# Performance work log

Hardware: AMD Instinct MI355X
Metric: run time of the kernel (lower is better)

The kernel has to match this reference:

```python
import jax, jax.numpy as jnp
import numpy as np

N_NODES = 100000
N_EDGES = 1600000
NEG_SLOPE = 0.2  # PyG GATConv default
BN_EPS = 1e-5


def gat_conv(x, src, dst, W, a_src, a_dst, bias):
    # x: [N, F], W: [F, H, C]
    h = jnp.einsum('nf,fhc->nhc', x, W)                 # [N, H, C]
    al_src = jnp.sum(h * a_src, axis=-1)                # [N, H]
    al_dst = jnp.sum(h * a_dst, axis=-1)                # [N, H]
    e = al_src[src] + al_dst[dst]                       # [E, H]
    e = jnp.where(e >= 0, e, NEG_SLOPE * e)             # leaky_relu(0.2)
    # segment softmax over incoming edges of each dst node
    emax = jax.ops.segment_max(e, dst, num_segments=N_NODES)
    ee = jnp.exp(e - emax[dst])
    denom = jax.ops.segment_sum(ee, dst, num_segments=N_NODES)
    alpha = ee / denom[dst]                             # [E, H]
    msg = alpha[:, :, None] * h[src]                    # [E, H, C]
    out = jax.ops.segment_sum(msg, dst, num_segments=N_NODES)  # [N, H, C]
    return out.mean(axis=1) + bias                      # concat=False -> head mean


def batch_norm(x, gamma, beta):
    mu = jnp.mean(x, axis=0)
    var = jnp.var(x, axis=0)  # biased, as in torch BN normalization
    return (x - mu) * jax.lax.rsqrt(var + BN_EPS) * gamma + beta


def setup_inputs() -> dict:
    key = jax.random.key(0)
    ks = jax.random.split(key, 16)
    inp = {
        'x': jax.random.normal(ks[0], (N_NODES, 128), jnp.float32),
        'edge_index': jax.random.randint(ks[1], (2, N_EDGES), 0, N_NODES, jnp.int64)
            if jax.config.jax_enable_x64 else
            jax.random.randint(ks[1], (2, N_EDGES), 0, N_NODES, jnp.int32),
        'edge_attr': jax.random.normal(ks[2], (N_EDGES, 8), jnp.float32),
        'W0': 0.1 * jax.random.normal(ks[3], (128, 4, 32), jnp.float32),
        'a_src0': 0.1 * jax.random.normal(ks[4], (4, 32), jnp.float32),
        'a_dst0': 0.1 * jax.random.normal(ks[5], (4, 32), jnp.float32),
        'b0': jnp.zeros((32,), jnp.float32),
        'g0': jnp.ones((32,), jnp.float32),
        'be0': jnp.zeros((32,), jnp.float32),
        'W1': 0.1 * jax.random.normal(ks[6], (32, 4, 32), jnp.float32),
        'a_src1': 0.1 * jax.random.normal(ks[7], (4, 32), jnp.float32),
        'a_dst1': 0.1 * jax.random.normal(ks[8], (4, 32), jnp.float32),
        'b1': jnp.zeros((32,), jnp.float32),
        'g1': jnp.ones((32,), jnp.float32),
        'be1': jnp.zeros((32,), jnp.float32),
        'W2': 0.1 * jax.random.normal(ks[9], (32, 4, 32), jnp.float32),
        'a_src2': 0.1 * jax.random.normal(ks[10], (4, 32), jnp.float32),
        'a_dst2': 0.1 * jax.random.normal(ks[11], (4, 32), jnp.float32),
        'b2': jnp.zeros((32,), jnp.float32),
    }
    return inp


def reference(x, edge_index, edge_attr, W0, a_src0, a_dst0, b0, g0, be0,
              W1, a_src1, a_dst1, b1, g1, be1, W2, a_src2, a_dst2, b2):
    src, dst = edge_index[0], edge_index[1]
    h = gat_conv(x, src, dst, W0, a_src0, a_dst0, b0)
    h = jax.nn.relu(batch_norm(h, g0, be0))  # dropout = identity (deterministic ref)
    h = gat_conv(h, src, dst, W1, a_src1, a_dst1, b1)
    h = jax.nn.relu(batch_norm(h, g1, be1))
    h = gat_conv(h, src, dst, W2, a_src2, a_dst2, b2)
    return (h, edge_attr)
```

## Files before the change

kernel.cpp:

```cpp
#include <hip/hip_runtime.h>
#include <cstdio>
#include <cstdint>

#define LRELU 0.2f
#define BN_EPS 1e-5f

typedef short bf16x8 __attribute__((ext_vector_type(8)));
typedef float f32x4 __attribute__((ext_vector_type(4)));

__device__ inline unsigned short f2bf(float f) {
  unsigned int u = __float_as_uint(f);
  u += 0x7fffu + ((u >> 16) & 1u);
  return (unsigned short)(u >> 16);
}
__device__ inline float bf2f(unsigned short v) {
  return __uint_as_float(((unsigned int)v) << 16);
}
__device__ inline float bflo(unsigned int u) { return __uint_as_float(u << 16); }
__device__ inline float bfhi(unsigned int u) { return __uint_as_float(u & 0xffff0000u); }


__global__ __launch_bounds__(256) void k_bhist_copy(const int* __restrict__ dst,
                                                    int* __restrict__ bh,
                                                    const float4* __restrict__ ea,
                                                    float4* __restrict__ oea,
                                                    int E) {
  __shared__ int cnt[512];
  for (int b = threadIdx.x; b < 512; b += 256) cnt[b] = 0;
  __syncthreads();
  const int gid = blockIdx.x * blockDim.x + threadIdx.x;
  const int gstride = gridDim.x * blockDim.x;
  for (int i = gid; i < E; i += gstride) atomicAdd(&cnt[dst[i] >> 8], 1);
  const int n4 = E * 2;
  for (int i = gid; i < n4; i += gstride) oea[i] = ea[i];
  __syncthreads();
  for (int b = threadIdx.x; b < 512; b += 256)
    if (cnt[b]) atomicAdd(&bh[b], cnt[b]);
}

__global__ __launch_bounds__(512) void k_exscan(const int* __restrict__ bh,
                                                int* __restrict__ bstart,
                                                int* __restrict__ bcur, int n,
                                                int* __restrict__ offsN) {
  __shared__ int sh[512];
  const int t = threadIdx.x;
  int v = (t < n) ? bh[t] : 0;
  sh[t] = v;
  __syncthreads();
  for (int s = 1; s < 512; s <<= 1) {
    int u = (t >= s) ? sh[t - s] : 0;
    __syncthreads();
    sh[t] += u;
    __syncthreads();
  }
  if (t < n) {
    int ex = sh[t] - v;
    bstart[t] = ex;
    bcur[t] = ex;
  }
  if (t == n - 1) {
    bstart[n] = sh[t];
    *offsN = sh[t];
  }
}

__global__ __launch_bounds__(256) void k_bscatter(const int* __restrict__ src,
                                                  const int* __restrict__ dst,
                                                  int* __restrict__ bcur,
                                                  uint2* __restrict__ bpair, int E) {
  __shared__ int cnt[512];
  const int chunk = (E + gridDim.x - 1) / gridDim.x;
  const int beg = blockIdx.x * chunk;
  const int end = min(E, beg + chunk);
  for (int b = threadIdx.x; b < 512; b += 256) cnt[b] = 0;
  __syncthreads();
  for (int e = beg + threadIdx.x; e < end; e += 256)
    atomicAdd(&cnt[dst[e] >> 8], 1);
  __syncthreads();
  for (int b = threadIdx.x; b < 512; b += 256) {
    int c = cnt[b];
    cnt[b] = (c > 0) ? atomicAdd(&bcur[b], c) : 0;
  }
  __syncthreads();
  for (int e = beg + threadIdx.x; e < end; e += 256) {
    int d = dst[e];
    int pos = atomicAdd(&cnt[d >> 8], 1);
    bpair[pos] = make_uint2((unsigned)src[e], (unsigned)d);
  }
}

__global__ __launch_bounds__(256) void k_bcsr2(const uint2* __restrict__ bpair,
                                               const int* __restrict__ bstart,
                                               int* __restrict__ offs,
                                               int* __restrict__ srcs, int N) {
  __shared__ int sc[256];
  __shared__ int cur[256];
  const int b = blockIdx.x;
  const int lo = b << 8;
  const int t = threadIdx.x;
  const int e0 = bstart[b], e1 = bstart[b + 1];
  sc[t] = 0;
  __syncthreads();
  for (int e = e0 + t; e < e1; e += 256) atomicAdd(&sc[bpair[e].y & 255], 1);
  __syncthreads();
  int v = sc[t];
  for (int s = 1; s < 256; s <<= 1) {
    int u = (t >= s) ? sc[t - s] : 0;
    __syncthreads();
    sc[t] += u;
    __syncthreads();
  }
  const int pos0 = e0 + sc[t] - v;
  cur[t] = pos0;
  if (lo + t < N) offs[lo + t] = pos0;
  __syncthreads();
  for (int e = e0 + t; e < e1; e += 256) {
    uint2 p = bpair[e];
    int pos = atomicAdd(&cur[p.y & 255], 1);
    srcs[pos] = (int)p.x;
  }
}

__global__ void k_castW3(const float* __restrict__ W0, const float* __restrict__ W1,
                         const float* __restrict__ W2,
                         unsigned short* __restrict__ Wt0,
                         unsigned short* __restrict__ Wt1,
                         unsigned short* __restrict__ Wt2) {
  int o = blockIdx.x * 256 + threadIdx.x;
  if (o < 16384) {
    int n = o >> 7, k = o & 127;
    Wt0[o] = f2bf(W0[k * 128 + n]);
  } else if (o < 20480) {
    int p = o - 16384, n = p >> 5, k = p & 31;
    Wt1[p] = f2bf(W1[k * 128 + n]);
  } else if (o < 24576) {
    int p = o - 20480, n = p >> 5, k = p & 31;
    Wt2[p] = f2bf(W2[k * 128 + n]);
  }
}

template <int K, bool BN>
__global__ __launch_bounds__(256) void k_mfma(
    const float* __restrict__ Ain, const unsigned short* __restrict__ Wt,
    const float* __restrict__ asrc, const float* __restrict__ adst,
    const float* __restrict__ stats, const float* __restrict__ g,
    const float* __restrict__ be,
    unsigned short* __restrict__ h, float* __restrict__ als,
    float* __restrict__ ald, int N) {
  __shared__ unsigned short lsh[4][16 * 132];
  __shared__ float sc_s[32], sh_s[32];
  const int wv   = threadIdx.x >> 6;
  const int lane = threadIdx.x & 63;
  const int quad = lane >> 4;
  const int col  = lane & 15;
  const int m0   = blockIdx.x * 64 + wv * 16;
  const int rowc = min(m0 + col, N - 1);

  if constexpr (BN) {
    if (threadIdx.x < 32) {
      float s = 0.f, ss = 0.f;
#pragma unroll
      for (int r = 0; r < 8; r++) {
        s  += stats[r * 64 + threadIdx.x];
        ss += stats[r * 64 + 32 + threadIdx.x];
      }
      const float inv = 1.f / (float)N;
      const float mu = s * inv;
      const float var = ss * inv - mu * mu;
      const float scv = g[threadIdx.x] * rsqrtf(var + BN_EPS);
      sc_s[threadIdx.x] = scv;
      sh_s[threadIdx.x] = be[threadIdx.x] - mu * scv;
    }
    __syncthreads();
  }

  f32x4 acc[8];
#pragma unroll
  for (int t = 0; t < 8; t++) acc[t] = (f32x4){0.f, 0.f, 0.f, 0.f};

#pragma unroll
  for (int ks = 0; ks < K / 32; ks++) {
    const int k0 = ks * 32 + quad * 8;
    const float* ap = Ain + (size_t)rowc * K + k0;
    float4 f0 = *(const float4*)ap;
    float4 f1 = *(const float4*)(ap + 4);
    bf16x8 a;
    if constexpr (BN) {
      f0.x = fmaxf(0.f, fmaf(f0.x, sc_s[k0 + 0], sh_s[k0 + 0]));
      f0.y = fmaxf(0.f, fmaf(f0.y, sc_s[k0 + 1], sh_s[k0 + 1]));
      f0.z = fmaxf(0.f, fmaf(f0.z, sc_s[k0 + 2], sh_s[k0 + 2]));
      f0.w = fmaxf(0.f, fmaf(f0.w, sc_s[k0 + 3], sh_s[k0 + 3]));
      f1.x = fmaxf(0.f, fmaf(f1.x, sc_s[k0 + 4], sh_s[k0 + 4]));
      f1.y = fmaxf(0.f, fmaf(f1.y, sc_s[k0 + 5], sh_s[k0 + 5]));
      f1.z = fmaxf(0.f, fmaf(f1.z, sc_s[k0 + 6], sh_s[k0 + 6]));
      f1.w = fmaxf(0.f, fmaf(f1.w, sc_s[k0 + 7], sh_s[k0 + 7]));
    }
    a[0] = (short)f2bf(f0.x); a[1] = (short)f2bf(f0.y);
    a[2] = (short)f2bf(f0.z); a[3] = (short)f2bf(f0.w);
    a[4] = (short)f2bf(f1.x); a[5] = (short)f2bf(f1.y);
    a[6] = (short)f2bf(f1.z); a[7] = (short)f2bf(f1.w);
#pragma unroll
    for (int t = 0; t < 8; t++) {
      bf16x8 b = *(const bf16x8*)(Wt + (size_t)(t * 16 + col) * K + k0);
      acc[t] = __builtin_amdgcn_mfma_f32_16x16x32_bf16(a, b, acc[t], 0, 0, 0);
    }
  }

#pragma unroll
  for (int t = 0; t < 8; t++) {
#pragma unroll
    for (int j = 0; j < 4; j++)
      lsh[wv][(quad * 4 + j) * 132 + col + 16 * t] = f2bf(acc[t][j]);
  }
  __syncthreads();

  float as8[8], ad8[8];
#pragma unroll
  for (int j = 0; j < 8; j++) {
    as8[j] = asrc[col * 8 + j];
    ad8[j] = adst[col * 8 + j];
  }

#pragma unroll
  for (int i = 0; i < 4; i++) {
    const int row = i * 4 + quad;
    const int hrow = m0 + row;
    const unsigned short* rp = &lsh[wv][row * 132 + col * 8];
    ushort4 lo = *(const ushort4*)rp;
    ushort4 hi = *(const ushort4*)(rp + 4);
    float p = 0.f, q = 0.f, v;
    v = bf2f(lo.x); p += v * as8[0]; q += v * ad8[0];
    v = bf2f(lo.y); p += v * as8[1]; q += v * ad8[1];
    v = bf2f(lo.z); p += v * as8[2]; q += v * ad8[2];
    v = bf2f(lo.w); p += v * as8[3]; q += v * ad8[3];
    v = bf2f(hi.x); p += v * as8[4]; q += v * ad8[4];
    v = bf2f(hi.y); p += v * as8[5]; q += v * ad8[5];
    v = bf2f(hi.z); p += v * as8[6]; q += v * ad8[6];
    v = bf2f(hi.w); p += v * as8[7]; q += v * ad8[7];
    if (hrow < N) {
      ushort4* gp = (ushort4*)(h + (size_t)hrow * 128 + col * 8);
      gp[0] = lo; gp[1] = hi;
    }
    p += __shfl_xor(p, 1); p += __shfl_xor(p, 2);
    q += __shfl_xor(q, 1); q += __shfl_xor(q, 2);
    if ((lane & 3) == 0 && hrow < N) {
      const int head = col >> 2;
      als[hrow * 4 + head] = p;
      ald[hrow * 4 + head] = q;
    }
  }
}

template <bool STATS>
__global__ __launch_bounds__(256) void k_agg(
    const unsigned int* __restrict__ h2, const float* __restrict__ als,
    const float* __restrict__ ald, const int* __restrict__ offs,
    const int* __restrict__ srcs, const float* __restrict__ bias,
    float* __restrict__ y, float* __restrict__ stats, int N) {
  __shared__ float s1[32], s2[32];
  const int node = blockIdx.x * 4 + (threadIdx.x >> 6);
  const int lane = threadIdx.x & 63;
  const bool valid = node < N;
  if constexpr (STATS) {
    if (threadIdx.x < 32) { s1[threadIdx.x] = 0.f; s2[threadIdx.x] = 0.f; }
    __syncthreads();
  } else {
    if (!valid) return;
  }

  if (valid) {
    const int half = lane >> 5;
    const int sub  = lane & 31;
    const int head = sub >> 3;
    const int beg = __builtin_amdgcn_readfirstlane(offs[node]);
    const int end = __builtin_amdgcn_readfirstlane(offs[node + 1]);
    const float ad = ald[node * 4 + head];
    float ax0 = 0.f, ax1 = 0.f, ax2 = 0.f, ax3 = 0.f, dn = 0.f;

    for (int base = beg; base < end; base += 64) {
      const int m = min(64, end - base);
      const int sv = srcs[base + min(lane, m - 1)];
      int j = 0;

#define PAIR(J)                                                            \
  {                                                                        \
    const int sA = __builtin_amdgcn_readlane(sv, (J));                     \
    const int sB = __builtin_amdgcn_readlane(sv, (J) + 1);                 \
    const int s = half ? sB : sA;                                          \
    const float a = als[s * 4 + head];                                     \
    const uint2 u = *(const uint2*)(h2 + (size_t)s * 64 + (sub << 1));     \
    float e = a + ad;                                                      \
    e = fmaxf(e, LRELU * e);                                               \
    const float w = __expf(e);                                             \
    dn += w;                                                               \
    ax0 = fmaf(w, bflo(u.x), ax0);                                         \
    ax1 = fmaf(w, bfhi(u.x), ax1);                                         \
    ax2 = fmaf(w, bflo(u.y), ax2);                                         \
    ax3 = fmaf(w, bfhi(u.y), ax3);                                         \
  }

      for (; j + 8 <= m; j += 8) {
        PAIR(j) PAIR(j + 2) PAIR(j + 4) PAIR(j + 6)
      }
      for (; j + 2 <= m; j += 2) { PAIR(j) }
      if (j < m) {
        const int s = __builtin_amdgcn_readlane(sv, j);
        const float a = als[s * 4 + head];
        const uint2 u = *(const uint2*)(h2 + (size_t)s * 64 + (sub << 1));
        float e = a + ad;
        e = fmaxf(e, LRELU * e);
        const float w = half ? 0.f : __expf(e);
        dn += w;
        ax0 = fmaf(w, bflo(u.x), ax0);
        ax1 = fmaf(w, bfhi(u.x), ax1);
        ax2 = fmaf(w, bflo(u.y), ax2);
        ax3 = fmaf(w, bfhi(u.y), ax3);
      }
#undef PAIR
    }

    dn += __shfl_xor(dn, 32);
    const float r = (dn > 0.f) ? (1.f / dn) : 0.f;
    ax0 *= r; ax1 *= r; ax2 *= r; ax3 *= r;
    ax0 += __shfl_xor(ax0, 32); ax1 += __shfl_xor(ax1, 32);
    ax2 += __shfl_xor(ax2, 32); ax3 += __shfl_xor(ax3, 32);
    ax0 += __shfl_xor(ax0, 8);  ax1 += __shfl_xor(ax1, 8);
    ax2 += __shfl_xor(ax2, 8);  ax3 += __shfl_xor(ax3, 8);
    ax0 += __shfl_xor(ax0, 16); ax1 += __shfl_xor(ax1, 16);
    ax2 += __shfl_xor(ax2, 16); ax3 += __shfl_xor(ax3, 16);

    if (lane < 8) {
      float4 b4 = ((const float4*)bias)[lane];
      float4 o;
      o.x = 0.25f * ax0 + b4.x;
      o.y = 0.25f * ax1 + b4.y;
      o.z = 0.25f * ax2 + b4.z;
      o.w = 0.25f * ax3 + b4.w;
      ((float4*)(y + (size_t)node * 32))[lane] = o;
      if constexpr (STATS) {
        atomicAdd(&s1[4 * lane + 0], o.x); atomicAdd(&s2[4 * lane + 0], o.x * o.x);
        atomicAdd(&s1[4 * lane + 1], o.y); atomicAdd(&s2[4 * lane + 1], o.y * o.y);
        atomicAdd(&s1[4 * lane + 2], o.z); atomicAdd(&s2[4 * lane + 2], o.z * o.z);
        atomicAdd(&s1[4 * lane + 3], o.w); atomicAdd(&s2[4 * lane + 3], o.w * o.w);
      }
    }
  }

  if constexpr (STATS) {
    __syncthreads();
    if (threadIdx.x < 32) {
      float* sb = stats + (blockIdx.x & 7) * 64;
      atomicAdd(&sb[threadIdx.x], s1[threadIdx.x]);
      atomicAdd(&sb[32 + threadIdx.x], s2[threadIdx.x]);
    }
  }
}

extern "C" void kernel_launch(void* const* d_in, const int* in_sizes, int n_in,
                              void* d_out, int out_size, void* d_ws, size_t ws_size,
                              hipStream_t stream) {
  const float* x   = (const float*)d_in[0];
  const int*   ei  = (const int*)d_in[1];
  const float* ea  = (const float*)d_in[2];
  const float* W0  = (const float*)d_in[3];
  const float* as0 = (const float*)d_in[4];
  const float* ad0 = (const float*)d_in[5];
  const float* b0  = (const float*)d_in[6];
  const float* g0  = (const float*)d_in[7];
  const float* be0 = (const float*)d_in[8];
  const float* W1  = (const float*)d_in[9];
  const float* as1 = (const float*)d_in[10];
  const float* ad1 = (const float*)d_in[11];
  const float* b1  = (const float*)d_in[12];
  const float* g1  = (const float*)d_in[13];
  const float* be1 = (const float*)d_in[14];
  const float* W2  = (const float*)d_in[15];
  const float* as2 = (const float*)d_in[16];
  const float* ad2 = (const float*)d_in[17];
  const float* b2  = (const float*)d_in[18];

  const int N = in_sizes[0] / 128;
  const int E = in_sizes[1] / 2;
  const int* srcI = ei;
  const int* dstI = ei + E;
  const int NB = (N + 255) >> 8;

  char* w = (char*)d_ws;
  auto carve = [&](size_t bytes) -> void* {
    void* p = (void*)w;
    w += (bytes + 255) & ~(size_t)255;
    return p;
  };
  unsigned short* h  = (unsigned short*)carve((size_t)N * 128 * 2);
  float* als        = (float*)carve((size_t)N * 4 * 4);
  float* ald        = (float*)carve((size_t)N * 4 * 4);
  float* y          = (float*)carve((size_t)N * 32 * 4);
  int* offs         = (int*)carve((size_t)(N + 1) * 4);
  int* srcs         = (int*)carve((size_t)E * 4);
  int* bh           = (int*)carve(512 * 4);
  float* stats      = (float*)carve(1024 * 4);
  char* zend        = w;
  int* bstart       = (int*)carve(513 * 4);
  int* bcur         = (int*)carve(512 * 4);
  unsigned short* Wt0 = (unsigned short*)carve(128 * 128 * 2);
  unsigned short* Wt1 = (unsigned short*)carve(128 * 32 * 2);
  unsigned short* Wt2 = (unsigned short*)carve(128 * 32 * 2);
  if ((size_t)(w - (char*)d_ws) > ws_size) {
    fprintf(stderr, "GAT kernel: ws too small (%zu needed, %zu given)\n",
            (size_t)(w - (char*)d_ws), ws_size);
    return;
  }
  uint2* bpair = (uint2*)h;

  float* out_nodes = (float*)d_out;
  float* out_ea    = out_nodes + (size_t)N * 32;

  hipMemsetAsync(bh, 0, (size_t)(zend - (char*)bh), stream);

  k_bhist_copy<<<256, 256, 0, stream>>>(dstI, bh, (const float4*)ea,
                                        (float4*)out_ea, E);
  k_exscan<<<1, 512, 0, stream>>>(bh, bstart, bcur, NB, offs + N);
  k_bscatter<<<128, 256, 0, stream>>>(srcI, dstI, bcur, bpair, E);
  k_bcsr2<<<NB, 256, 0, stream>>>(bpair, bstart, offs, srcs, N);

  k_castW3<<<96, 256, 0, stream>>>(W0, W1, W2, Wt0, Wt1, Wt2);

  const int gGemm = (N + 63) / 64;
  const int gAgg  = (N + 3) / 4;

  k_mfma<128, false><<<gGemm, 256, 0, stream>>>(x, Wt0, as0, ad0,
                                                nullptr, nullptr, nullptr,
                                                h, als, ald, N);
  k_agg<true><<<gAgg, 256, 0, stream>>>((const unsigned int*)h, als, ald, offs,
                                        srcs, b0, y, stats, N);
  k_mfma<32, true><<<gGemm, 256, 0, stream>>>(y, Wt1, as1, ad1, stats, g0, be0,
                                              h, als, ald, N);
  k_agg<true><<<gAgg, 256, 0, stream>>>((const unsigned int*)h, als, ald, offs,
                                        srcs, b1, y, stats + 512, N);
  k_mfma<32, true><<<gGemm, 256, 0, stream>>>(y, Wt2, as2, ad2, stats + 512, g1, be1,
                                              h, als, ald, N);
  k_agg<false><<<gAgg, 256, 0, stream>>>((const unsigned int*)h, als, ald, offs,
                                         srcs, b2, out_nodes, nullptr, N);
}
```

Baseline: 615.9 us.

## Slice h features into per-head column slabs and split aggregation into sliced gather plus reduce

The GEMM now writes h in eight column slices of 16 bf16 values, each stored contiguously across all nodes, and writes attention logits head-major. A new gather kernel processes one slice per block, so the gathered working set per slice is smaller and more cache-resident. A separate reduce kernel sums the four heads and adds bias and BN stats. The cost is an extra fp32 intermediate of N×128 values written and read back, plus three more kernel launches, and each edge's source index and logits are now reloaded once per slice.

After: 1.174 ms. 90.6% more time.

```diff
diff --git a/kernel.cpp b/kernel.cpp
--- a/kernel.cpp
+++ b/kernel.cpp
@@ -7,6 +7,7 @@
 
 typedef short bf16x8 __attribute__((ext_vector_type(8)));
 typedef float f32x4 __attribute__((ext_vector_type(4)));
+typedef float f32x2 __attribute__((ext_vector_type(2)));
 
 __device__ inline unsigned short f2bf(float f) {
   unsigned int u = __float_as_uint(f);
@@ -238,114 +239,115 @@
     v = bf2f(hi.z); p += v * as8[6]; q += v * ad8[6];
     v = bf2f(hi.w); p += v * as8[7]; q += v * ad8[7];
     if (hrow < N) {
-      ushort4* gp = (ushort4*)(h + (size_t)hrow * 128 + col * 8);
-      gp[0] = lo; gp[1] = hi;
+      const int qs = col >> 1;
+      unsigned short* gp = h + (size_t)qs * N * 16 + (size_t)hrow * 16 + (col & 1) * 8;
+      ((ushort4*)gp)[0] = lo;
+      ((ushort4*)gp)[1] = hi;
     }
     p += __shfl_xor(p, 1); p += __shfl_xor(p, 2);
     q += __shfl_xor(q, 1); q += __shfl_xor(q, 2);
     if ((lane & 3) == 0 && hrow < N) {
       const int head = col >> 2;
-      als[hrow * 4 + head] = p;
-      ald[hrow * 4 + head] = q;
+      als[(size_t)head * N + hrow] = p;
+      ald[(size_t)head * N + hrow] = q;
+    }
+  }
+}
+
+#define NPB 16
+__global__ __launch_bounds__(256) void k_gat(
+    const unsigned int* __restrict__ hs,
+    const float* __restrict__ alsh,
+    const float* __restrict__ aldh,
+    const int* __restrict__ offs,
+    const int* __restrict__ srcs,
+    float* __restrict__ ysl,
+    int N) {
+  const int slice = blockIdx.x & 7;
+  const int head  = slice >> 1;
+  const int chunk = blockIdx.x >> 3;
+  const int wv    = threadIdx.x >> 6;
+  const int lane  = threadIdx.x & 63;
+  const int slot  = lane >> 3;
+  const int chp   = lane & 7;
+  const unsigned int* __restrict__ hb = hs + (size_t)slice * N * 8;
+  const float* __restrict__ alh = alsh + (size_t)head * N;
+  float* __restrict__ yb = ysl + (size_t)slice * N * 16;
+
+  for (int ni = 0; ni < 4; ni++) {
+    const int node = chunk * NPB + wv * 4 + ni;
+    if (node >= N) break;
+    const int beg = __builtin_amdgcn_readfirstlane(offs[node]);
+    const int end = __builtin_amdgcn_readfirstlane(offs[node + 1]);
+    const float ad = aldh[(size_t)head * N + node];
+    float a0 = 0.f, a1 = 0.f, dn = 0.f;
+
+    for (int base = beg; base < end; base += 64) {
+      const int m = min(64, end - base);
+      const int sv = __builtin_nontemporal_load(&srcs[base + min(lane, m - 1)]);
+      for (int j0 = 0; j0 < m; j0 += 8) {
+        const int j = j0 + slot;
+        const int s = __shfl(sv, min(j, m - 1));
+        const float al = alh[s];
+        const unsigned int u = hb[(size_t)s * 8 + chp];
+        float e = al + ad;
+        e = fmaxf(e, LRELU * e);
+        float w = __expf(e);
+        w = (j < m) ? w : 0.f;
+        dn += w;
+        a0 = fmaf(w, bflo(u), a0);
+        a1 = fmaf(w, bfhi(u), a1);
+      }
+    }
+    dn += __shfl_xor(dn, 8);  a0 += __shfl_xor(a0, 8);  a1 += __shfl_xor(a1, 8);
+    dn += __shfl_xor(dn, 16); a0 += __shfl_xor(a0, 16); a1 += __shfl_xor(a1, 16);
+    dn += __shfl_xor(dn, 32); a0 += __shfl_xor(a0, 32); a1 += __shfl_xor(a1, 32);
+    if (lane < 8) {
+      const float r = (dn > 0.f) ? (1.f / dn) : 0.f;
+      f32x2 o;
+      o[0] = a0 * r;
+      o[1] = a1 * r;
+      __builtin_nontemporal_store(o, (f32x2*)(yb + (size_t)node * 16 + chp * 2));
     }
   }
 }
 
 template <bool STATS>
-__global__ __launch_bounds__(256) void k_agg(
-    const unsigned int* __restrict__ h2, const float* __restrict__ als,
-    const float* __restrict__ ald, const int* __restrict__ offs,
-    const int* __restrict__ srcs, const float* __restrict__ bias,
+__global__ __launch_bounds__(256) void k_red(
+    const float* __restrict__ ysl, const float* __restrict__ bias,
     float* __restrict__ y, float* __restrict__ stats, int N) {
   __shared__ float s1[32], s2[32];
-  const int node = blockIdx.x * 4 + (threadIdx.x >> 6);
-  const int lane = threadIdx.x & 63;
-  const bool valid = node < N;
   if constexpr (STATS) {
     if (threadIdx.x < 32) { s1[threadIdx.x] = 0.f; s2[threadIdx.x] = 0.f; }
     __syncthreads();
-  } else {
-    if (!valid) return;
-  }
-
-  if (valid) {
-    const int half = lane >> 5;
-    const int sub  = lane & 31;
-    const int head = sub >> 3;
-    const int beg = __builtin_amdgcn_readfirstlane(offs[node]);
-    const int end = __builtin_amdgcn_readfirstlane(offs[node + 1]);
-    const float ad = ald[node * 4 + head];
-    float ax0 = 0.f, ax1 = 0.f, ax2 = 0.f, ax3 = 0.f, dn = 0.f;
-
-    for (int base = beg; base < end; base += 64) {
-      const int m = min(64, end - base);
-      const int sv = srcs[base + min(lane, m - 1)];
-      int j = 0;
-
-#define PAIR(J)                                                            \
-  {                                                                        \
-    const int sA = __builtin_amdgcn_readlane(sv, (J));                     \
-    const int sB = __builtin_amdgcn_readlane(sv, (J) + 1);                 \
-    const int s = half ? sB : sA;                                          \
-    const float a = als[s * 4 + head];                                     \
-    const uint2 u = *(const uint2*)(h2 + (size_t)s * 64 + (sub << 1));     \
-    float e = a + ad;                                                      \
-    e = fmaxf(e, LRELU * e);                                               \
-    const float w = __expf(e);                                             \
-    dn += w;                                                               \
-    ax0 = fmaf(w, bflo(u.x), ax0);                                         \
-    ax1 = fmaf(w, bfhi(u.x), ax1);                                         \
-    ax2 = fmaf(w, bflo(u.y), ax2);                                         \
-    ax3 = fmaf(w, bfhi(u.y), ax3);                                         \
-  }
-
-      for (; j + 8 <= m; j += 8) {
-        PAIR(j) PAIR(j + 2) PAIR(j + 4) PAIR(j + 6)
-      }
-      for (; j + 2 <= m; j += 2) { PAIR(j) }
-      if (j < m) {
-        const int s = __builtin_amdgcn_readlane(sv, j);
-        const float a = als[s * 4 + head];
-        const uint2 u = *(const uint2*)(h2 + (size_t)s * 64 + (sub << 1));
-        float e = a + ad;
-        e = fmaxf(e, LRELU * e);
-        const float w = half ? 0.f : __expf(e);
-        dn += w;
-        ax0 = fmaf(w, bflo(u.x), ax0);
-        ax1 = fmaf(w, bfhi(u.x), ax1);
-        ax2 = fmaf(w, bflo(u.y), ax2);
-        ax3 = fmaf(w, bfhi(u.y), ax3);
-      }
-#undef PAIR
-    }
-
-    dn += __shfl_xor(dn, 32);
-    const float r = (dn > 0.f) ? (1.f / dn) : 0.f;
-    ax0 *= r; ax1 *= r; ax2 *= r; ax3 *= r;
-    ax0 += __shfl_xor(ax0, 32); ax1 += __shfl_xor(ax1, 32);
-    ax2 += __shfl_xor(ax2, 32); ax3 += __shfl_xor(ax3, 32);
-    ax0 += __shfl_xor(ax0, 8);  ax1 += __shfl_xor(ax1, 8);
-    ax2 += __shfl_xor(ax2, 8);  ax3 += __shfl_xor(ax3, 8);
-    ax0 += __shfl_xor(ax0, 16); ax1 += __shfl_xor(ax1, 16);
-    ax2 += __shfl_xor(ax2, 16); ax3 += __shfl_xor(ax3, 16);
-
-    if (lane < 8) {
-      float4 b4 = ((const float4*)bias)[lane];
-      float4 o;
-      o.x = 0.25f * ax0 + b4.x;
-      o.y = 0.25f * ax1 + b4.y;
-      o.z = 0.25f * ax2 + b4.z;
-      o.w = 0.25f * ax3 + b4.w;
-      ((float4*)(y + (size_t)node * 32))[lane] = o;
-      if constexpr (STATS) {
-        atomicAdd(&s1[4 * lane + 0], o.x); atomicAdd(&s2[4 * lane + 0], o.x * o.x);
-        atomicAdd(&s1[4 * lane + 1], o.y); atomicAdd(&s2[4 * lane + 1], o.y * o.y);
-        atomicAdd(&s1[4 * lane + 2], o.z); atomicAdd(&s2[4 * lane + 2], o.z * o.z);
-        atomicAdd(&s1[4 * lane + 3], o.w); atomicAdd(&s2[4 * lane + 3], o.w * o.w);
-      }
-    }
-  }
-
+  }
+  const int gidx = blockIdx.x * 256 + threadIdx.x;
+  const int node = gidx >> 3;
+  const int cg = gidx & 7;
+  if (node < N) {
+    const int hi = cg >> 2;
+    const int off = (cg & 3) * 4;
+    float4 s = {0.f, 0.f, 0.f, 0.f};
+#pragma unroll
+    for (int hh = 0; hh < 4; hh++) {
+      const float4 p = *(const float4*)(ysl +
+          ((size_t)(hh * 2 + hi) * N + node) * 16 + off);
+      s.x += p.x; s.y += p.y; s.z += p.z; s.w += p.w;
+    }
+    const float4 b4 = *(const float4*)(bias + cg * 4);
+    float4 o;
+    o.x = 0.25f * s.x + b4.x;
+    o.y = 0.25f * s.y + b4.y;
+    o.z = 0.25f * s.z + b4.z;
+    o.w = 0.25f * s.w + b4.w;
+    *(float4*)(y + (size_t)node * 32 + cg * 4) = o;
+    if constexpr (STATS) {
+      atomicAdd(&s1[cg * 4 + 0], o.x); atomicAdd(&s2[cg * 4 + 0], o.x * o.x);
+      atomicAdd(&s1[cg * 4 + 1], o.y); atomicAdd(&s2[cg * 4 + 1], o.y * o.y);
+      atomicAdd(&s1[cg * 4 + 2], o.z); atomicAdd(&s2[cg * 4 + 2], o.z * o.z);
+      atomicAdd(&s1[cg * 4 + 3], o.w); atomicAdd(&s2[cg * 4 + 3], o.w * o.w);
+    }
+  }
   if constexpr (STATS) {
     __syncthreads();
     if (threadIdx.x < 32) {
@@ -395,6 +397,7 @@
   float* als        = (float*)carve((size_t)N * 4 * 4);
   float* ald        = (float*)carve((size_t)N * 4 * 4);
   float* y          = (float*)carve((size_t)N * 32 * 4);
+  float* ysl        = (float*)carve((size_t)N * 8 * 16 * 4);
   int* offs         = (int*)carve((size_t)(N + 1) * 4);
   int* srcs         = (int*)carve((size_t)E * 4);
   int* bh           = (int*)carve(512 * 4);
@@ -415,7 +418,7 @@
   float* out_nodes = (float*)d_out;
   float* out_ea    = out_nodes + (size_t)N * 32;
 
-  hipMemsetAsync(bh, 0, (size_t)(zend - (char*)bh), stream);
+  (void)hipMemsetAsync(bh, 0, (size_t)(zend - (char*)bh), stream);
 
   k_bhist_copy<<<256, 256, 0, stream>>>(dstI, bh, (const float4*)ea,
                                         (float4*)out_ea, E);
@@ -426,19 +429,23 @@
   k_castW3<<<96, 256, 0, stream>>>(W0, W1, W2, Wt0, Wt1, Wt2);
 
   const int gGemm = (N + 63) / 64;
-  const int gAgg  = (N + 3) / 4;
+  const int gGat  = 8 * ((N + NPB - 1) / NPB);
+  const int gRed  = (N * 8 + 255) / 256;
 
   k_mfma<128, false><<<gGemm, 256, 0, stream>>>(x, Wt0, as0, ad0,
                                                 nullptr, nullptr, nullptr,
                                                 h, als, ald, N);
-  k_agg<true><<<gAgg, 256, 0, stream>>>((const unsigned int*)h, als, ald, offs,
-                                        srcs, b0, y, stats, N);
+  k_gat<<<gGat, 256, 0, stream>>>((const unsigned int*)h, als, ald, offs, srcs,
+                                  ysl, N);
+  k_red<true><<<gRed, 256, 0, stream>>>(ysl, b0, y, stats, N);
   k_mfma<32, true><<<gGemm, 256, 0, stream>>>(y, Wt1, as1, ad1, stats, g0, be0,
                                               h, als, ald, N);
-  k_agg<true><<<gAgg, 256, 0, stream>>>((const unsigned int*)h, als, ald, offs,
-                                        srcs, b1, y, stats + 512, N);
+  k_gat<<<gGat, 256, 0, stream>>>((const unsigned int*)h, als, ald, offs, srcs,
+                                  ysl, N);
+  k_red<true><<<gRed, 256, 0, stream>>>(ysl, b1, y, stats + 512, N);
   k_mfma<32, true><<<gGemm, 256, 0, stream>>>(y, Wt2, as2, ad2, stats + 512, g1, be1,
                                               h, als, ald, N);
-  k_agg<false><<<gAgg, 256, 0, stream>>>((const unsigned int*)h, als, ald, offs,
-                                         srcs, b2, out_nodes, nullptr, N);
-}
+  k_gat<<<gGat, 256, 0, stream>>>((const unsigned int*)h, als, ald, offs, srcs,
+                                  ysl, N);
+  k_red<false><<<gRed, 256, 0, stream>>>(ysl, b2, out_nodes, nullptr, N);
+}
```
